# Optimization experiments

Measured on AMD Instinct MI355X. Metric: run time of the kernel, lower is better.

## Reference

```python
import jax, jax.numpy as jnp
import numpy as np

NUM_EMBEDDINGS = 4096
LATENT_DIM = 256
COMMITMENT_COST = 0.25


def setup_inputs() -> dict:
    key = jax.random.key(0)
    k1, k2 = jax.random.split(key)
    x = jax.random.normal(k1, (8, 16, 256, LATENT_DIM), dtype=jnp.float32)
    # codebook initialized uniform(-1/K, 1/K) as in the torch module
    codebook = jax.random.uniform(
        k2, (NUM_EMBEDDINGS, LATENT_DIM), dtype=jnp.float32,
        minval=-1.0 / NUM_EMBEDDINGS, maxval=1.0 / NUM_EMBEDDINGS)
    return {"x": x, "codebook": codebook}


def reference(x, codebook):
    B, T, P, D = x.shape
    z_e = x.reshape(B * T * P, D)                      # [N, D]
    # squared L2 distances: ||z||^2 + ||e||^2 - 2 z.e  -> [N, K]
    z_sq = jnp.sum(z_e * z_e, axis=-1, keepdims=True)  # [N, 1]
    e_sq = jnp.sum(codebook * codebook, axis=-1)       # [K]
    distances = z_sq + e_sq - 2.0 * (z_e @ codebook.T)
    encoding_indices = jnp.argmin(distances, axis=-1)  # [N] int32
    z_q = codebook[encoding_indices].reshape(B, T, P, D)
    # codebook loss + commitment loss (mean squared error)
    loss = jnp.mean((z_q - jax.lax.stop_gradient(x)) ** 2) \
         + COMMITMENT_COST * jnp.mean((jax.lax.stop_gradient(z_q) - x) ** 2)
    # straight-through estimator
    z_q_st = x + jax.lax.stop_gradient(z_q - x)
    return z_q_st, loss, encoding_indices
```

## Files before the change

### kernel.cpp

```cpp
#include <hip/hip_runtime.h>

typedef __attribute__((ext_vector_type(8))) short bf16x8;
typedef __attribute__((ext_vector_type(4))) float f32x4;

#define DIMD 256
#define KCODES 4096
#define NROWS 32768
#define OUT_LOSS 8388608
#define OUT_IDX  8388609
#define MAXC 8
#define EPSQ 40u
#define QSCALE 273066.67f
#define QBIAS  0.12f

struct CandEntry { int row; int cnt; int codes[MAXC]; };

#define WS_CLIST 4096u
#define CCAP     16384
#define WS_OVF   659456u
#define OVFCAP   8192
#define WS_BSW   (1024u*1024u)
#define WS_END   (WS_BSW + (unsigned)KCODES*DIMD*2u)

#define SROWS      128
#define SMEM_WIDX  98816
#define SMEM_WPART 99328
#define SMEM_BYTES 99360

__device__ __forceinline__ unsigned short bf16_rne(float f) {
    unsigned u = __float_as_uint(f);
    u += 0x7FFFu + ((u >> 16) & 1u);
    return (unsigned short)(u >> 16);
}

__device__ __forceinline__ unsigned med3u(unsigned a, unsigned b, unsigned c) {
    unsigned d;
    asm("v_med3_u32 %0, %1, %2, %3" : "=v"(d) : "v"(a), "v"(b), "v"(c));
    return d;
}

__global__ void init_kernel(float* __restrict__ loss_acc, int* __restrict__ wcount,
                            int* __restrict__ ovfcount) {
    if (threadIdx.x == 0) { loss_acc[0] = 0.0f; wcount[0] = 0; ovfcount[0] = 0; }
}

__global__ __launch_bounds__(256) void convertB_kernel(const float* __restrict__ src,
                                                       unsigned short* __restrict__ bsw,
                                                       float* __restrict__ loss_acc,
                                                       int* __restrict__ wcount,
                                                       int* __restrict__ ovfcount,
                                                       int* __restrict__ done) {
    if (blockIdx.x == 0 && threadIdx.x == 0) {
        loss_acc[0] = 0.0f; wcount[0] = 0; ovfcount[0] = 0; done[0] = 0;
    }
    const unsigned u = blockIdx.x * 256 + threadIdx.x;
    const int laneq = u & 3;
    const int kc    = (u >> 2) & 7;
    const int c     = u >> 5;
    const float4 f0 = *(const float4*)(src + (size_t)c * DIMD + kc * 32 + laneq * 8);
    const float4 f1 = *(const float4*)(src + (size_t)c * DIMD + kc * 32 + laneq * 8 + 4);
    ushort4 h0, h1;
    h0.x = bf16_rne(f0.x); h0.y = bf16_rne(f0.y); h0.z = bf16_rne(f0.z); h0.w = bf16_rne(f0.w);
    h1.x = bf16_rne(f1.x); h1.y = bf16_rne(f1.y); h1.z = bf16_rne(f1.z); h1.w = bf16_rne(f1.w);
    const int g = c >> 4, lanem = c & 15;
    unsigned short* dst = bsw + ((size_t)((g * 8 + kc) * 64 + lanem * 4 + laneq)) * 8;
    *(ushort4*)(dst) = h0;
    *(ushort4*)(dst + 4) = h1;
}

__global__ __launch_bounds__(512, 2) void vq_screen_kernel(
        const unsigned short* __restrict__ Bsw,
        const float* __restrict__ x, const float* __restrict__ cb,
        float* __restrict__ out, float* __restrict__ loss_acc,
        int* __restrict__ wcount, CandEntry* __restrict__ clist,
        int* __restrict__ ovfcount, int* __restrict__ ovflist) {
    __shared__ __align__(16) char smem[SMEM_BYTES];
    unsigned short* Asw = (unsigned short*)smem;
    unsigned* keys = (unsigned*)smem;
    int*   widx  = (int*)(smem + SMEM_WIDX);
    float* wpart = (float*)(smem + SMEM_WPART);

    const int tid   = threadIdx.x;
    const int wv    = tid >> 6;
    const int rh    = wv >> 2;
    const int w4    = wv & 3;
    const int lane  = tid & 63;
    const int lanem = lane & 15;
    const int laneq = lane >> 4;
    const int rb    = blockIdx.x * SROWS;
    const int phase = blockIdx.x & 31;

    #pragma unroll
    for (int q = 0; q < 8; ++q) {
        const unsigned u = q * 512 + tid;
        const int lq = u & 3;
        const int kc = (u >> 2) & 7;
        const int rr = u >> 5;
        const float* srcp = x + (size_t)(rb + rr) * DIMD + kc * 32 + lq * 8;
        const float4 f0 = *(const float4*)(srcp);
        const float4 f1 = *(const float4*)(srcp + 4);
        bf16x8 v;
        v[0] = (short)bf16_rne(f0.x); v[1] = (short)bf16_rne(f0.y);
        v[2] = (short)bf16_rne(f0.z); v[3] = (short)bf16_rne(f0.w);
        v[4] = (short)bf16_rne(f1.x); v[5] = (short)bf16_rne(f1.y);
        v[6] = (short)bf16_rne(f1.z); v[7] = (short)bf16_rne(f1.w);
        const int i = rr >> 4, lm = rr & 15;
        *(bf16x8*)(Asw + ((size_t)((i * 8 + kc) * 64 + lq * 16 + lm)) * 8) = v;
    }
    __syncthreads();

    bf16x8 ah[2][8];
    #pragma unroll
    for (int i = 0; i < 2; ++i)
        #pragma unroll
        for (int kc = 0; kc < 8; ++kc)
            ah[i][kc] = *(const bf16x8*)(Asw + (size_t)(((rh * 4 + i) * 8 + kc) * 64 + lane) * 8);

    unsigned b1[16], b2[16], b3[16];
    #pragma unroll
    for (int s = 0; s < 16; ++s) { b1[s] = 0xFFFFFFFFu; b2[s] = 0xFFFFFFFFu; b3[s] = 0xFFFFFFFFu; }

    const int loff = (lanem * 4 + laneq) * 8;

#define LOADH(dst, ctv, jv)                                                       \
    do {                                                                          \
        const int g_ = (ctv) * 8 + w4 * 2 + (jv);                                 \
        _Pragma("unroll")                                                         \
        for (int kc_ = 0; kc_ < 8; ++kc_)                                         \
            dst[kc_] = *(const bf16x8*)(Bsw + (size_t)(g_ * 8 + kc_) * 512 + loff); \
    } while (0)

    bf16x8 bA[8], bB[8];
    LOADH(bA, phase, 0);
    LOADH(bB, phase, 1);

    for (int ct = 0; ct < KCODES / 128; ++ct) {
        const int ctp = (ct + phase) & 31;
        const int ctn = (ctp + 1) & 31;
        f32x4 acc0[4], acc1[4];
        #pragma unroll
        for (int i = 0; i < 4; ++i) {
            acc0[i] = (f32x4){0.f, 0.f, 0.f, 0.f};
            acc1[i] = (f32x4){0.f, 0.f, 0.f, 0.f};
        }

        const int gA = ctn * 8 + w4 * 2 + 0;
        const int gB = ctn * 8 + w4 * 2 + 1;

        #pragma unroll
        for (int kc = 0; kc < 8; ++kc) {
            const bf16x8 a2k = *(const bf16x8*)(Asw + (size_t)(((rh * 4 + 2) * 8 + kc) * 64 + lane) * 8);
            const bf16x8 a3k = *(const bf16x8*)(Asw + (size_t)(((rh * 4 + 3) * 8 + kc) * 64 + lane) * 8);
            acc0[0] = __builtin_amdgcn_mfma_f32_16x16x32_bf16(ah[0][kc], bA[kc], acc0[0], 0, 0, 0);
            acc1[0] = __builtin_amdgcn_mfma_f32_16x16x32_bf16(ah[0][kc], bB[kc], acc1[0], 0, 0, 0);
            acc0[1] = __builtin_amdgcn_mfma_f32_16x16x32_bf16(ah[1][kc], bA[kc], acc0[1], 0, 0, 0);
            acc1[1] = __builtin_amdgcn_mfma_f32_16x16x32_bf16(ah[1][kc], bB[kc], acc1[1], 0, 0, 0);
            acc0[2] = __builtin_amdgcn_mfma_f32_16x16x32_bf16(a2k, bA[kc], acc0[2], 0, 0, 0);
            acc1[2] = __builtin_amdgcn_mfma_f32_16x16x32_bf16(a2k, bB[kc], acc1[2], 0, 0, 0);
            acc0[3] = __builtin_amdgcn_mfma_f32_16x16x32_bf16(a3k, bA[kc], acc0[3], 0, 0, 0);
            acc1[3] = __builtin_amdgcn_mfma_f32_16x16x32_bf16(a3k, bB[kc], acc1[3], 0, 0, 0);
            bA[kc] = *(const bf16x8*)(Bsw + (size_t)(gA * 8 + kc) * 512 + loff);
            bB[kc] = *(const bf16x8*)(Bsw + (size_t)(gB * 8 + kc) * 512 + loff);
            __builtin_amdgcn_sched_barrier(0x38F);
        }

        {
            const unsigned code = (unsigned)(ctp * 128 + w4 * 32 + lanem);
            #pragma unroll
            for (int i = 0; i < 4; ++i)
                #pragma unroll
                for (int r = 0; r < 4; ++r) {
                    const int s = i * 4 + r;
                    const float dist = fmaf(acc0[i][r], -2.0f * QSCALE, QBIAS * QSCALE);
                    const unsigned k = ((unsigned)dist << 12) | code;
                    const unsigned nb1 = min(b1[s], k);
                    const unsigned nb2 = med3u(b1[s], b2[s], k);
                    const unsigned nb3 = med3u(b2[s], b3[s], k);
                    b1[s] = nb1; b2[s] = nb2; b3[s] = nb3;
                }
        }
        {
            const unsigned code = (unsigned)(ctp * 128 + w4 * 32 + 16 + lanem);
            #pragma unroll
            for (int i = 0; i < 4; ++i)
                #pragma unroll
                for (int r = 0; r < 4; ++r) {
                    const int s = i * 4 + r;
                    const float dist = fmaf(acc1[i][r], -2.0f * QSCALE, QBIAS * QSCALE);
                    const unsigned k = ((unsigned)dist << 12) | code;
                    const unsigned nb1 = min(b1[s], k);
                    const unsigned nb2 = med3u(b1[s], b2[s], k);
                    const unsigned nb3 = med3u(b2[s], b3[s], k);
                    b1[s] = nb1; b2[s] = nb2; b3[s] = nb3;
                }
        }
    }
#undef LOADH

    __syncthreads();

    {
        const int src = w4 * 16 + lanem;
        #pragma unroll
        for (int i = 0; i < 4; ++i)
            #pragma unroll
            for (int r = 0; r < 4; ++r) {
                const int s = i * 4 + r;
                const int rr = rh * 64 + i * 16 + laneq * 4 + r;
                keys[rr * 193 + src * 3 + 0] = b1[s];
                keys[rr * 193 + src * 3 + 1] = b2[s];
                keys[rr * 193 + src * 3 + 2] = b3[s];
            }
    }
    __syncthreads();
    if (tid < SROWS) {
        const int base = tid * 193;
        unsigned kmin = 0xFFFFFFFFu;
        for (int t = 0; t < 192; ++t) kmin = min(kmin, keys[base + t]);
        const unsigned thr = (((kmin >> 12) + EPSQ) << 12) | 0xFFFu;
        int cand[MAXC]; int nc = 0; int ovf = 0;
        for (int L = 0; L < 64; ++L) {
            const unsigned v0 = keys[base + L * 3 + 0];
            if (v0 <= thr) {
                if (nc < MAXC) cand[nc] = (int)(v0 & 0xFFFu);
                ++nc;
                const unsigned v1 = keys[base + L * 3 + 1];
                if (v1 <= thr) {
                    if (nc < MAXC) cand[nc] = (int)(v1 & 0xFFFu);
                    ++nc;
                    const unsigned v2 = keys[base + L * 3 + 2];
                    if (v2 <= thr) {
                        if (nc < MAXC) cand[nc] = (int)(v2 & 0xFFFu);
                        ++nc;
                        ovf = 1;
                    }
                }
            }
        }
        const int row = rb + tid;
        const int bi = (int)(kmin & 0xFFFu);
        widx[tid] = bi;
        out[OUT_IDX + (size_t)row] = (float)bi;
        if (ovf || nc > MAXC) {
            const int op = atomicAdd(ovfcount, 1);
            if (op < OVFCAP) ovflist[op] = row;
        } else if (nc >= 2) {
            const int pos = atomicAdd(wcount, 1);
            if (pos < CCAP) {
                CandEntry* e = &clist[pos];
                e->row = row; e->cnt = nc;
                for (int q = 0; q < nc; ++q) e->codes[q] = cand[q];
            } else {
                const int op = atomicAdd(ovfcount, 1);
                if (op < OVFCAP) ovflist[op] = row;
            }
        }
    }
    __syncthreads();

    float lsum = 0.0f;
    const int dv = (tid & 63) * 4;
    const int rs = tid >> 6;
    const float* xblk = x + (size_t)rb * DIMD;
    float* oblk = out + (size_t)rb * DIMD;
    for (int p = 0; p < 16; ++p) {
        const int row = p * 8 + rs;
        const int wi = widx[row];
        float4 xv = *(const float4*)(xblk + (size_t)row * DIMD + dv);
        float4 cv = *(const float4*)(cb + (size_t)wi * DIMD + dv);
        const float d0 = cv.x - xv.x, d1 = cv.y - xv.y, d2 = cv.z - xv.z, d3 = cv.w - xv.w;
        float4 o;
        o.x = xv.x + d0; o.y = xv.y + d1; o.z = xv.z + d2; o.w = xv.w + d3;
        *(float4*)(oblk + (size_t)row * DIMD + dv) = o;
        lsum += d0 * d0 + d1 * d1 + d2 * d2 + d3 * d3;
    }
    #pragma unroll
    for (int off = 32; off > 0; off >>= 1) lsum += __shfl_down(lsum, off, 64);
    if ((tid & 63) == 0) wpart[tid >> 6] = lsum;
    __syncthreads();
    if (tid == 0) {
        float t = 0.0f;
        #pragma unroll
        for (int i = 0; i < 8; ++i) t += wpart[i];
        atomicAdd(loss_acc, t);
    }
}

__global__ __launch_bounds__(256) void vq_fix_kernel(
        const float* __restrict__ x, const float* __restrict__ cb,
        float* __restrict__ out, float* __restrict__ loss_acc,
        const int* __restrict__ wcount, const CandEntry* __restrict__ clist,
        const int* __restrict__ ovfcount, const int* __restrict__ ovflist,
        int* __restrict__ done) {
    __shared__ double xd[DIMD];
    __shared__ double zred[256];
    __shared__ float  rdq[256];
    __shared__ int    ri[256];
    __shared__ float  lred[256];
    const int tid = threadIdx.x;

    {
        int count = wcount[0];
        if (count > CCAP) count = CCAP;
        const int lane = tid & 63;
        const int gw = blockIdx.x * 4 + (tid >> 6);
        const int nw = gridDim.x * 4;
        for (int it = gw; it < count; it += nw) {
            const CandEntry* e = clist + it;
            const int row = e->row;
            const int cnt = e->cnt;
            const float4 xv = *(const float4*)(x + (size_t)row * DIMD + lane * 4);
            double zs = (double)xv.x * xv.x + (double)xv.y * xv.y
                      + (double)xv.z * xv.z + (double)xv.w * xv.w;
            #pragma unroll
            for (int off = 32; off > 0; off >>= 1) zs += __shfl_xor(zs, off, 64);
            const float Zf = (float)zs;
            float bq = 3.4e38f; int bi = 0x7fffffff;
            for (int q = 0; q < cnt; ++q) {
                const int c = e->codes[q];
                const float4 cv = *(const float4*)(cb + (size_t)c * DIMD + lane * 4);
                double dp = (double)xv.x * cv.x + (double)xv.y * cv.y
                          + (double)xv.z * cv.z + (double)xv.w * cv.w;
                #pragma unroll
                for (int off = 32; off > 0; off >>= 1) dp += __shfl_xor(dp, off, 64);
                const float wv = (float)(2.0 * dp);
                const float dq = Zf - wv;
                if (dq < bq || (dq == bq && c < bi)) { bq = dq; bi = c; }
            }
            const int oldi = (int)out[OUT_IDX + (size_t)row];
            if (bi != oldi) {
                const float4 cn = *(const float4*)(cb + (size_t)bi * DIMD + lane * 4);
                const float4 co = *(const float4*)(cb + (size_t)oldi * DIMD + lane * 4);
                float4 o; float ls = 0.0f;
                { const float dn = cn.x - xv.x, dd = co.x - xv.x; o.x = xv.x + dn; ls += dn*dn - dd*dd; }
                { const float dn = cn.y - xv.y, dd = co.y - xv.y; o.y = xv.y + dn; ls += dn*dn - dd*dd; }
                { const float dn = cn.z - xv.z, dd = co.z - xv.z; o.z = xv.z + dn; ls += dn*dn - dd*dd; }
                { const float dn = cn.w - xv.w, dd = co.w - xv.w; o.w = xv.w + dn; ls += dn*dn - dd*dd; }
                *(float4*)(out + (size_t)row * DIMD + lane * 4) = o;
                #pragma unroll
                for (int off = 32; off > 0; off >>= 1) ls += __shfl_xor(ls, off, 64);
                if (lane == 0) {
                    atomicAdd(loss_acc, ls);
                    out[OUT_IDX + (size_t)row] = (float)bi;
                }
            }
        }
    }

    __syncthreads();
    {
        int count = ovfcount[0];
        if (count > OVFCAP) count = OVFCAP;
        for (int item = blockIdx.x; item < count; item += gridDim.x) {
            const int row = ovflist[item];
            const double xv0 = (double)x[(size_t)row * DIMD + tid];
            xd[tid] = xv0;
            zred[tid] = xv0 * xv0;
            __syncthreads();
            for (int st = 128; st > 0; st >>= 1) {
                if (tid < st) zred[tid] += zred[tid + st];
                __syncthreads();
            }
            const float Zf = (float)zred[0];
            float bq = 3.4e38f; int bi = 0x7fffffff;
            for (int q = 0; q < 16; ++q) {
                const int c = q * 256 + tid;
                const float* cr = cb + (size_t)c * DIMD;
                double s0 = 0.0, s1 = 0.0, s2 = 0.0, s3 = 0.0;
                #pragma unroll 4
                for (int d = 0; d < DIMD; d += 16) {
                    float4 c0 = *(const float4*)(cr + d);
                    float4 c1 = *(const float4*)(cr + d + 4);
                    float4 c2 = *(const float4*)(cr + d + 8);
                    float4 c3 = *(const float4*)(cr + d + 12);
                    s0 += xd[d + 0] * (double)c0.x + xd[d + 1] * (double)c0.y
                        + xd[d + 2] * (double)c0.z + xd[d + 3] * (double)c0.w;
                    s1 += xd[d + 4] * (double)c1.x + xd[d + 5] * (double)c1.y
                        + xd[d + 6] * (double)c1.z + xd[d + 7] * (double)c1.w;
                    s2 += xd[d + 8] * (double)c2.x + xd[d + 9] * (double)c2.y
                        + xd[d +10] * (double)c2.z + xd[d +11] * (double)c2.w;
                    s3 += xd[d +12] * (double)c3.x + xd[d +13] * (double)c3.y
                        + xd[d +14] * (double)c3.z + xd[d +15] * (double)c3.w;
                }
                const double s = (s0 + s1) + (s2 + s3);
                const float wv = (float)(2.0 * s);
                const float dq = Zf - wv;
                if (dq < bq || (dq == bq && c < bi)) { bq = dq; bi = c; }
            }
            rdq[tid] = bq; ri[tid] = bi;
            __syncthreads();
            for (int st = 128; st > 0; st >>= 1) {
                if (tid < st) {
                    const float oq = rdq[tid + st]; const int oi = ri[tid + st];
                    if (oq < rdq[tid] || (oq == rdq[tid] && oi < ri[tid])) {
                        rdq[tid] = oq; ri[tid] = oi;
                    }
                }
                __syncthreads();
            }
            const int newi = ri[0];
            const int oldi = (int)out[OUT_IDX + (size_t)row];
            if (newi != oldi) {
                const float xv = x[(size_t)row * DIMD + tid];
                const float co = cb[(size_t)oldi * DIMD + tid];
                const float cn = cb[(size_t)newi * DIMD + tid];
                const float dold = co - xv, dnew = cn - xv;
                out[(size_t)row * DIMD + tid] = xv + dnew;
                lred[tid] = dnew * dnew - dold * dold;
            } else {
                lred[tid] = 0.0f;
            }
            __syncthreads();
            for (int st = 128; st > 0; st >>= 1) {
                if (tid < st) lred[tid] += lred[tid + st];
                __syncthreads();
            }
            if (tid == 0 && newi != oldi) {
                atomicAdd(loss_acc, lred[0]);
                out[OUT_IDX + (size_t)row] = (float)newi;
            }
            __syncthreads();
        }
    }

    __syncthreads();
    if (tid == 0) {
        __threadfence();
        const int t = atomicAdd(done, 1);
        if (t == (int)gridDim.x - 1) {
            __threadfence();
            out[OUT_LOSS] = 1.25f * (loss_acc[0] / 8388608.0f);
        }
    }
}

__global__ __launch_bounds__(256) void vq_ovf_kernel(
        const float* __restrict__ x, const float* __restrict__ cb,
        float* __restrict__ out, float* __restrict__ loss_acc,
        const int* __restrict__ ovfcount, const int* __restrict__ ovflist) {
    __shared__ double xd[DIMD];
    __shared__ double zred[256];
    __shared__ float  rdq[256];
    __shared__ int    ri[256];
    __shared__ float  lred[256];
    const int tid = threadIdx.x;
    int count = ovfcount[0];
    if (count > OVFCAP) count = OVFCAP;
    for (int item = blockIdx.x; item < count; item += gridDim.x) {
        const int row = ovflist[item];
        const double xv0 = (double)x[(size_t)row * DIMD + tid];
        xd[tid] = xv0;
        zred[tid] = xv0 * xv0;
        __syncthreads();
        for (int st = 128; st > 0; st >>= 1) {
            if (tid < st) zred[tid] += zred[tid + st];
            __syncthreads();
        }
        const float Zf = (float)zred[0];
        float bq = 3.4e38f; int bi = 0x7fffffff;
        for (int q = 0; q < 16; ++q) {
            const int c = q * 256 + tid;
            const float* cr = cb + (size_t)c * DIMD;
            double s0 = 0.0, s1 = 0.0, s2 = 0.0, s3 = 0.0;
            #pragma unroll 4
            for (int d = 0; d < DIMD; d += 16) {
                float4 c0 = *(const float4*)(cr + d);
                float4 c1 = *(const float4*)(cr + d + 4);
                float4 c2 = *(const float4*)(cr + d + 8);
                float4 c3 = *(const float4*)(cr + d + 12);
                s0 += xd[d + 0] * (double)c0.x + xd[d + 1] * (double)c0.y
                    + xd[d + 2] * (double)c0.z + xd[d + 3] * (double)c0.w;
                s1 += xd[d + 4] * (double)c1.x + xd[d + 5] * (double)c1.y
                    + xd[d + 6] * (double)c1.z + xd[d + 7] * (double)c1.w;
                s2 += xd[d + 8] * (double)c2.x + xd[d + 9] * (double)c2.y
                    + xd[d +10] * (double)c2.z + xd[d +11] * (double)c2.w;
                s3 += xd[d +12] * (double)c3.x + xd[d +13] * (double)c3.y
                    + xd[d +14] * (double)c3.z + xd[d +15] * (double)c3.w;
            }
            const double s = (s0 + s1) + (s2 + s3);
            const float wv = (float)(2.0 * s);
            const float dq = Zf - wv;
            if (dq < bq || (dq == bq && c < bi)) { bq = dq; bi = c; }
        }
        rdq[tid] = bq; ri[tid] = bi;
        __syncthreads();
        for (int st = 128; st > 0; st >>= 1) {
            if (tid < st) {
                const float oq = rdq[tid + st]; const int oi = ri[tid + st];
                if (oq < rdq[tid] || (oq == rdq[tid] && oi < ri[tid])) {
                    rdq[tid] = oq; ri[tid] = oi;
                }
            }
            __syncthreads();
        }
        const int newi = ri[0];
        const int oldi = (int)out[OUT_IDX + (size_t)row];
        if (newi != oldi) {
            const float xv = x[(size_t)row * DIMD + tid];
            const float co = cb[(size_t)oldi * DIMD + tid];
            const float cn = cb[(size_t)newi * DIMD + tid];
            const float dold = co - xv, dnew = cn - xv;
            out[(size_t)row * DIMD + tid] = xv + dnew;
            lred[tid] = dnew * dnew - dold * dold;
        } else {
            lred[tid] = 0.0f;
        }
        __syncthreads();
        for (int st = 128; st > 0; st >>= 1) {
            if (tid < st) lred[tid] += lred[tid + st];
            __syncthreads();
        }
        if (tid == 0 && newi != oldi) {
            atomicAdd(loss_acc, lred[0]);
            out[OUT_IDX + (size_t)row] = (float)newi;
        }
        __syncthreads();
    }
}

__global__ void finalize_kernel(const float* __restrict__ loss_acc, float* __restrict__ out) {
    if (threadIdx.x == 0 && blockIdx.x == 0)
        out[OUT_LOSS] = 1.25f * (loss_acc[0] / 8388608.0f);
}

#define MT 128
#define DK 32
#define LSTR 130
#define FLAG_EPS_F32 3.6e-5f
__global__ __launch_bounds__(256) void vq_main_fp32_kernel(const float* __restrict__ x,
                                                           const float* __restrict__ cb,
                                                           float* __restrict__ out,
                                                           float* __restrict__ loss_acc,
                                                           int* __restrict__ wcount,
                                                           int* __restrict__ wlist,
                                                           int wcap) {
    __shared__ float As[DK * LSTR];
    __shared__ float Bs[DK * LSTR];
    __shared__ float red_d[MT * 17];
    __shared__ float red_2[MT * 17];
    __shared__ int   red_i[MT * 17];
    __shared__ int   widx[MT];
    __shared__ float wpart[4];
    const int tid = threadIdx.x;
    const int tx = tid & 15;
    const int ty = tid >> 4;
    const float* xblk = x + (size_t)blockIdx.x * MT * DIMD;
    float b1[8], b2[8]; int i1[8];
    #pragma unroll
    for (int i = 0; i < 8; ++i) { b1[i] = 3.4e38f; b2[i] = 3.4e38f; i1[i] = 0; }
    const int sr = tid >> 3;
    const int sd = (tid & 7) * 4;
    for (int kt = 0; kt < KCODES; kt += 128) {
        float acc[8][8];
        #pragma unroll
        for (int i = 0; i < 8; ++i)
            #pragma unroll
            for (int j = 0; j < 8; ++j) acc[i][j] = 0.0f;
        const float* bblk = cb + (size_t)kt * DIMD;
        for (int dc = 0; dc < DIMD; dc += DK) {
            __syncthreads();
            #pragma unroll
            for (int p = 0; p < 4; ++p) {
                const int r = p * 32 + sr;
                float4 va = *(const float4*)(xblk + (size_t)r * DIMD + dc + sd);
                float4 vb = *(const float4*)(bblk + (size_t)r * DIMD + dc + sd);
                As[(sd + 0) * LSTR + r] = va.x; As[(sd + 1) * LSTR + r] = va.y;
                As[(sd + 2) * LSTR + r] = va.z; As[(sd + 3) * LSTR + r] = va.w;
                Bs[(sd + 0) * LSTR + r] = vb.x; Bs[(sd + 1) * LSTR + r] = vb.y;
                Bs[(sd + 2) * LSTR + r] = vb.z; Bs[(sd + 3) * LSTR + r] = vb.w;
            }
            __syncthreads();
            #pragma unroll 4
            for (int d = 0; d < DK; ++d) {
                const float2* ap = (const float2*)&As[d * LSTR + ty * 8];
                const float2* bp = (const float2*)&Bs[d * LSTR + tx * 8];
                float2 a0 = ap[0], a1 = ap[1], a2 = ap[2], a3 = ap[3];
                float2 c0 = bp[0], c1 = bp[1], c2 = bp[2], c3 = bp[3];
                float a[8] = {a0.x, a0.y, a1.x, a1.y, a2.x, a2.y, a3.x, a3.y};
                float b[8] = {c0.x, c0.y, c1.x, c1.y, c2.x, c2.y, c3.x, c3.y};
                #pragma unroll
                for (int i = 0; i < 8; ++i)
                    #pragma unroll
                    for (int j = 0; j < 8; ++j)
                        acc[i][j] += a[i] * b[j];
            }
        }
        #pragma unroll
        for (int j = 0; j < 8; ++j) {
            const int code = kt + tx * 8 + j;
            #pragma unroll
            for (int i = 0; i < 8; ++i) {
                const float dist = -(acc[i][j] + acc[i][j]);
                if (dist < b1[i]) { b2[i] = b1[i]; b1[i] = dist; i1[i] = code; }
                else if (dist < b2[i]) b2[i] = dist;
            }
        }
    }
    __syncthreads();
    #pragma unroll
    for (int i = 0; i < 8; ++i) {
        red_d[(ty * 8 + i) * 17 + tx] = b1[i];
        red_2[(ty * 8 + i) * 17 + tx] = b2[i];
        red_i[(ty * 8 + i) * 17 + tx] = i1[i];
    }
    __syncthreads();
    if (tid < MT) {
        float bd = red_d[tid * 17];
        float s2 = red_2[tid * 17];
        int   bi = red_i[tid * 17];
        #pragma unroll
        for (int t = 1; t < 16; ++t) {
            const float d1 = red_d[tid * 17 + t];
            const float d2 = red_2[tid * 17 + t];
            const int   ii = red_i[tid * 17 + t];
            if (d1 < bd || (d1 == bd && ii < bi)) { s2 = fminf(bd, d2); bd = d1; bi = ii; }
            else s2 = fminf(s2, d1);
        }
        const int row = blockIdx.x * MT + tid;
        widx[tid] = bi;
        out[OUT_IDX + (size_t)row] = (float)bi;
        if (s2 - bd <= FLAG_EPS_F32) {
            const int pos = atomicAdd(wcount, 1);
            if (pos < wcap) wlist[pos] = row;
        }
    }
    __syncthreads();
    float lsum = 0.0f;
    const int dv = (tid & 63) * 4;
    const int rs = tid >> 6;
    float* oblk = out + (size_t)blockIdx.x * MT * DIMD;
    for (int p = 0; p < 32; ++p) {
        const int row = p * 4 + rs;
        const int wi = widx[row];
        float4 xv = *(const float4*)(xblk + (size_t)row * DIMD + dv);
        float4 cv = *(const float4*)(cb + (size_t)wi * DIMD + dv);
        const float d0 = cv.x - xv.x, d1 = cv.y - xv.y, d2 = cv.z - xv.z, d3 = cv.w - xv.w;
        float4 o;
        o.x = xv.x + d0; o.y = xv.y + d1; o.z = xv.z + d2; o.w = xv.w + d3;
        *(float4*)(oblk + (size_t)row * DIMD + dv) = o;
        lsum += d0 * d0 + d1 * d1 + d2 * d2 + d3 * d3;
    }
    #pragma unroll
    for (int off = 32; off > 0; off >>= 1) lsum += __shfl_down(lsum, off, 64);
    if ((tid & 63) == 0) wpart[tid >> 6] = lsum;
    __syncthreads();
    if (tid == 0) atomicAdd(loss_acc, wpart[0] + wpart[1] + wpart[2] + wpart[3]);
}

extern "C" void kernel_launch(void* const* d_in, const int* in_sizes, int n_in,
                              void* d_out, int out_size, void* d_ws, size_t ws_size,
                              hipStream_t stream) {
    const float* x  = (const float*)d_in[0];
    const float* cb = (const float*)d_in[1];
    float* out = (float*)d_out;
    float* loss_acc = (float*)d_ws;
    int*   wcount   = (int*)((char*)d_ws + 32);
    int*   ovfcount = (int*)((char*)d_ws + 36);
    int*   done     = (int*)((char*)d_ws + 40);
    CandEntry* clist = (CandEntry*)((char*)d_ws + WS_CLIST);
    int*   ovflist  = (int*)((char*)d_ws + WS_OVF);

    if (ws_size >= (size_t)WS_END) {
        unsigned short* Bsw = (unsigned short*)((char*)d_ws + WS_BSW);
        convertB_kernel<<<512, 256, 0, stream>>>(cb, Bsw, loss_acc, wcount, ovfcount, done);
        vq_screen_kernel<<<256, 512, 0, stream>>>(Bsw, x, cb, out, loss_acc,
                                                  wcount, clist, ovfcount, ovflist);
        vq_fix_kernel<<<512, 256, 0, stream>>>(x, cb, out, loss_acc,
                                               wcount, clist, ovfcount, ovflist, done);
    } else {
        init_kernel<<<1, 64, 0, stream>>>(loss_acc, wcount, ovfcount);
        int* wlist = (int*)((char*)d_ws + WS_CLIST);
        int wcap = 0;
        if (ws_size > WS_CLIST + sizeof(int)) {
            size_t c = (ws_size - WS_CLIST) / sizeof(int);
            wcap = (int)(c > 32768 ? 32768 : c);
        }
        vq_main_fp32_kernel<<<256, 256, 0, stream>>>(x, cb, out, loss_acc,
                                                     wcount, wlist, wcap);
        vq_ovf_kernel<<<512, 256, 0, stream>>>(x, cb, out, loss_acc, wcount, wlist);
        finalize_kernel<<<1, 1, 0, stream>>>(loss_acc, out);
    }
}
```

Baseline: 193.7 us.

## Fuse candidate rescoring into screen kernel via shared-memory candidate list

The screen kernel now keeps ambiguous-row candidates in a per-block shared-memory list instead of a global list. After the main pass it rescores them in double precision inside the same block, using the indices held in shared memory. The old fix kernel is split, and only the overflow full-search and loss finalize remain in a separate kernel, launched with fewer blocks. This removes global atomics, candidate-list traffic and a heavy kernel stage. In exchange the screen kernel gets a serial tail and a little more shared memory, which may hurt occupancy.

```diff
diff --git a/kernel.cpp b/kernel.cpp
--- a/kernel.cpp
+++ b/kernel.cpp
@@ -25,7 +25,9 @@
 #define SROWS      128
 #define SMEM_WIDX  98816
 #define SMEM_WPART 99328
-#define SMEM_BYTES 99360
+#define SMEM_BCNT  99360
+#define SMEM_CAND  99376
+#define SMEM_BYTES (SMEM_CAND + 128 * 10 * 4)
 
 __device__ __forceinline__ unsigned short bf16_rne(float f) {
     unsigned u = __float_as_uint(f);
@@ -72,13 +74,14 @@
         const unsigned short* __restrict__ Bsw,
         const float* __restrict__ x, const float* __restrict__ cb,
         float* __restrict__ out, float* __restrict__ loss_acc,
-        int* __restrict__ wcount, CandEntry* __restrict__ clist,
         int* __restrict__ ovfcount, int* __restrict__ ovflist) {
     __shared__ __align__(16) char smem[SMEM_BYTES];
     unsigned short* Asw = (unsigned short*)smem;
     unsigned* keys = (unsigned*)smem;
     int*   widx  = (int*)(smem + SMEM_WIDX);
     float* wpart = (float*)(smem + SMEM_WPART);
+    int*   bcnt  = (int*)(smem + SMEM_BCNT);
+    int*   candL = (int*)(smem + SMEM_CAND);
 
     const int tid   = threadIdx.x;
     const int wv    = tid >> 6;
@@ -89,6 +92,8 @@
     const int laneq = lane >> 4;
     const int rb    = blockIdx.x * SROWS;
     const int phase = blockIdx.x & 31;
+
+    if (tid == 0) bcnt[0] = 0;
 
     #pragma unroll
     for (int q = 0; q < 8; ++q) {
@@ -245,15 +250,10 @@
             const int op = atomicAdd(ovfcount, 1);
             if (op < OVFCAP) ovflist[op] = row;
         } else if (nc >= 2) {
-            const int pos = atomicAdd(wcount, 1);
-            if (pos < CCAP) {
-                CandEntry* e = &clist[pos];
-                e->row = row; e->cnt = nc;
-                for (int q = 0; q < nc; ++q) e->codes[q] = cand[q];
-            } else {
-                const int op = atomicAdd(ovfcount, 1);
-                if (op < OVFCAP) ovflist[op] = row;
-            }
+            const int pos = atomicAdd(bcnt, 1);
+            int* e = candL + pos * 10;
+            e[0] = tid; e[1] = nc;
+            for (int q = 0; q < nc; ++q) e[2 + q] = cand[q];
         }
     }
     __syncthreads();
@@ -284,31 +284,15 @@
         for (int i = 0; i < 8; ++i) t += wpart[i];
         atomicAdd(loss_acc, t);
     }
-}
-
-__global__ __launch_bounds__(256) void vq_fix_kernel(
-        const float* __restrict__ x, const float* __restrict__ cb,
-        float* __restrict__ out, float* __restrict__ loss_acc,
-        const int* __restrict__ wcount, const CandEntry* __restrict__ clist,
-        const int* __restrict__ ovfcount, const int* __restrict__ ovflist,
-        int* __restrict__ done) {
-    __shared__ double xd[DIMD];
-    __shared__ double zred[256];
-    __shared__ float  rdq[256];
-    __shared__ int    ri[256];
-    __shared__ float  lred[256];
-    const int tid = threadIdx.x;
+    __syncthreads();
 
     {
-        int count = wcount[0];
-        if (count > CCAP) count = CCAP;
-        const int lane = tid & 63;
-        const int gw = blockIdx.x * 4 + (tid >> 6);
-        const int nw = gridDim.x * 4;
-        for (int it = gw; it < count; it += nw) {
-            const CandEntry* e = clist + it;
-            const int row = e->row;
-            const int cnt = e->cnt;
+        const int items = bcnt[0];
+        for (int it = wv; it < items; it += 8) {
+            const int* e = candL + it * 10;
+            const int r = e[0];
+            const int cnt = e[1];
+            const int row = rb + r;
             const float4 xv = *(const float4*)(x + (size_t)row * DIMD + lane * 4);
             double zs = (double)xv.x * xv.x + (double)xv.y * xv.y
                       + (double)xv.z * xv.z + (double)xv.w * xv.w;
@@ -317,17 +301,17 @@
             const float Zf = (float)zs;
             float bq = 3.4e38f; int bi = 0x7fffffff;
             for (int q = 0; q < cnt; ++q) {
-                const int c = e->codes[q];
+                const int c = e[2 + q];
                 const float4 cv = *(const float4*)(cb + (size_t)c * DIMD + lane * 4);
                 double dp = (double)xv.x * cv.x + (double)xv.y * cv.y
                           + (double)xv.z * cv.z + (double)xv.w * cv.w;
                 #pragma unroll
                 for (int off = 32; off > 0; off >>= 1) dp += __shfl_xor(dp, off, 64);
-                const float wv = (float)(2.0 * dp);
-                const float dq = Zf - wv;
+                const float wvv = (float)(2.0 * dp);
+                const float dq = Zf - wvv;
                 if (dq < bq || (dq == bq && c < bi)) { bq = dq; bi = c; }
             }
-            const int oldi = (int)out[OUT_IDX + (size_t)row];
+            const int oldi = widx[r];
             if (bi != oldi) {
                 const float4 cn = *(const float4*)(cb + (size_t)bi * DIMD + lane * 4);
                 const float4 co = *(const float4*)(cb + (size_t)oldi * DIMD + lane * 4);
@@ -346,84 +330,91 @@
             }
         }
     }
-
-    __syncthreads();
-    {
-        int count = ovfcount[0];
-        if (count > OVFCAP) count = OVFCAP;
-        for (int item = blockIdx.x; item < count; item += gridDim.x) {
-            const int row = ovflist[item];
-            const double xv0 = (double)x[(size_t)row * DIMD + tid];
-            xd[tid] = xv0;
-            zred[tid] = xv0 * xv0;
-            __syncthreads();
-            for (int st = 128; st > 0; st >>= 1) {
-                if (tid < st) zred[tid] += zred[tid + st];
-                __syncthreads();
-            }
-            const float Zf = (float)zred[0];
-            float bq = 3.4e38f; int bi = 0x7fffffff;
-            for (int q = 0; q < 16; ++q) {
-                const int c = q * 256 + tid;
-                const float* cr = cb + (size_t)c * DIMD;
-                double s0 = 0.0, s1 = 0.0, s2 = 0.0, s3 = 0.0;
-                #pragma unroll 4
-                for (int d = 0; d < DIMD; d += 16) {
-                    float4 c0 = *(const float4*)(cr + d);
-                    float4 c1 = *(const float4*)(cr + d + 4);
-                    float4 c2 = *(const float4*)(cr + d + 8);
-                    float4 c3 = *(const float4*)(cr + d + 12);
-                    s0 += xd[d + 0] * (double)c0.x + xd[d + 1] * (double)c0.y
-                        + xd[d + 2] * (double)c0.z + xd[d + 3] * (double)c0.w;
-                    s1 += xd[d + 4] * (double)c1.x + xd[d + 5] * (double)c1.y
-                        + xd[d + 6] * (double)c1.z + xd[d + 7] * (double)c1.w;
-                    s2 += xd[d + 8] * (double)c2.x + xd[d + 9] * (double)c2.y
-                        + xd[d +10] * (double)c2.z + xd[d +11] * (double)c2.w;
-                    s3 += xd[d +12] * (double)c3.x + xd[d +13] * (double)c3.y
-                        + xd[d +14] * (double)c3.z + xd[d +15] * (double)c3.w;
+}
+
+__global__ __launch_bounds__(256) void vq_ovffin_kernel(
+        const float* __restrict__ x, const float* __restrict__ cb,
+        float* __restrict__ out, float* __restrict__ loss_acc,
+        const int* __restrict__ ovfcount, const int* __restrict__ ovflist,
+        int* __restrict__ done) {
+    __shared__ double xd[DIMD];
+    __shared__ double zred[256];
+    __shared__ float  rdq[256];
+    __shared__ int    ri[256];
+    __shared__ float  lred[256];
+    const int tid = threadIdx.x;
+    int count = ovfcount[0];
+    if (count > OVFCAP) count = OVFCAP;
+    for (int item = blockIdx.x; item < count; item += gridDim.x) {
+        const int row = ovflist[item];
+        const double xv0 = (double)x[(size_t)row * DIMD + tid];
+        xd[tid] = xv0;
+        zred[tid] = xv0 * xv0;
+        __syncthreads();
+        for (int st = 128; st > 0; st >>= 1) {
+            if (tid < st) zred[tid] += zred[tid + st];
+            __syncthreads();
+        }
+        const float Zf = (float)zred[0];
+        float bq = 3.4e38f; int bi = 0x7fffffff;
+        for (int q = 0; q < 16; ++q) {
+            const int c = q * 256 + tid;
+            const float* cr = cb + (size_t)c * DIMD;
+            double s0 = 0.0, s1 = 0.0, s2 = 0.0, s3 = 0.0;
+            #pragma unroll 4
+            for (int d = 0; d < DIMD; d += 16) {
+                float4 c0 = *(const float4*)(cr + d);
+                float4 c1 = *(const float4*)(cr + d + 4);
+                float4 c2 = *(const float4*)(cr + d + 8);
+                float4 c3 = *(const float4*)(cr + d + 12);
+                s0 += xd[d + 0] * (double)c0.x + xd[d + 1] * (double)c0.y
+                    + xd[d + 2] * (double)c0.z + xd[d + 3] * (double)c0.w;
+                s1 += xd[d + 4] * (double)c1.x + xd[d + 5] * (double)c1.y
+                    + xd[d + 6] * (double)c1.z + xd[d + 7] * (double)c1.w;
+                s2 += xd[d + 8] * (double)c2.x + xd[d + 9] * (double)c2.y
+                    + xd[d +10] * (double)c2.z + xd[d +11] * (double)c2.w;
+                s3 += xd[d +12] * (double)c3.x + xd[d +13] * (double)c3.y
+                    + xd[d +14] * (double)c3.z + xd[d +15] * (double)c3.w;
+            }
+            const double s = (s0 + s1) + (s2 + s3);
+            const float wv = (float)(2.0 * s);
+            const float dq = Zf - wv;
+            if (dq < bq || (dq == bq && c < bi)) { bq = dq; bi = c; }
+        }
+        rdq[tid] = bq; ri[tid] = bi;
+        __syncthreads();
+        for (int st = 128; st > 0; st >>= 1) {
+            if (tid < st) {
+                const float oq = rdq[tid + st]; const int oi = ri[tid + st];
+                if (oq < rdq[tid] || (oq == rdq[tid] && oi < ri[tid])) {
+                    rdq[tid] = oq; ri[tid] = oi;
                 }
-                const double s = (s0 + s1) + (s2 + s3);
-                const float wv = (float)(2.0 * s);
-                const float dq = Zf - wv;
-                if (dq < bq || (dq == bq && c < bi)) { bq = dq; bi = c; }
-            }
-            rdq[tid] = bq; ri[tid] = bi;
-            __syncthreads();
-            for (int st = 128; st > 0; st >>= 1) {
-                if (tid < st) {
-                    const float oq = rdq[tid + st]; const int oi = ri[tid + st];
-                    if (oq < rdq[tid] || (oq == rdq[tid] && oi < ri[tid])) {
-                        rdq[tid] = oq; ri[tid] = oi;
-                    }
-                }
-                __syncthreads();
-            }
-            const int newi = ri[0];
-            const int oldi = (int)out[OUT_IDX + (size_t)row];
-            if (newi != oldi) {
-                const float xv = x[(size_t)row * DIMD + tid];
-                const float co = cb[(size_t)oldi * DIMD + tid];
-                const float cn = cb[(size_t)newi * DIMD + tid];
-                const float dold = co - xv, dnew = cn - xv;
-                out[(size_t)row * DIMD + tid] = xv + dnew;
-                lred[tid] = dnew * dnew - dold * dold;
-            } else {
-                lred[tid] = 0.0f;
-            }
-            __syncthreads();
-            for (int st = 128; st > 0; st >>= 1) {
-                if (tid < st) lred[tid] += lred[tid + st];
-                __syncthreads();
-            }
-            if (tid == 0 && newi != oldi) {
-                atomicAdd(loss_acc, lred[0]);
-                out[OUT_IDX + (size_t)row] = (float)newi;
-            }
-            __syncthreads();
-        }
-    }
-
-    __syncthreads();
+            }
+            __syncthreads();
+        }
+        const int newi = ri[0];
+        const int oldi = (int)out[OUT_IDX + (size_t)row];
+        if (newi != oldi) {
+            const float xv = x[(size_t)row * DIMD + tid];
+            const float co = cb[(size_t)oldi * DIMD + tid];
+            const float cn = cb[(size_t)newi * DIMD + tid];
+            const float dold = co - xv, dnew = cn - xv;
+            out[(size_t)row * DIMD + tid] = xv + dnew;
+            lred[tid] = dnew * dnew - dold * dold;
+        } else {
+            lred[tid] = 0.0f;
+        }
+        __syncthreads();
+        for (int st = 128; st > 0; st >>= 1) {
+            if (tid < st) lred[tid] += lred[tid + st];
+            __syncthreads();
+        }
+        if (tid == 0 && newi != oldi) {
+            atomicAdd(loss_acc, lred[0]);
+            out[OUT_IDX + (size_t)row] = (float)newi;
+        }
+        __syncthreads();
+    }
     if (tid == 0) {
         __threadfence();
         const int t = atomicAdd(done, 1);
@@ -657,16 +648,15 @@
     int*   wcount   = (int*)((char*)d_ws + 32);
     int*   ovfcount = (int*)((char*)d_ws + 36);
     int*   done     = (int*)((char*)d_ws + 40);
-    CandEntry* clist = (CandEntry*)((char*)d_ws + WS_CLIST);
     int*   ovflist  = (int*)((char*)d_ws + WS_OVF);
 
     if (ws_size >= (size_t)WS_END) {
         unsigned short* Bsw = (unsigned short*)((char*)d_ws + WS_BSW);
         convertB_kernel<<<512, 256, 0, stream>>>(cb, Bsw, loss_acc, wcount, ovfcount, done);
         vq_screen_kernel<<<256, 512, 0, stream>>>(Bsw, x, cb, out, loss_acc,
-                                                  wcount, clist, ovfcount, ovflist);
-        vq_fix_kernel<<<512, 256, 0, stream>>>(x, cb, out, loss_acc,
-                                               wcount, clist, ovfcount, ovflist, done);
+                                                  ovfcount, ovflist);
+        vq_ovffin_kernel<<<256, 256, 0, stream>>>(x, cb, out, loss_acc,
+                                                  ovfcount, ovflist, done);
     } else {
         init_kernel<<<1, 64, 0, stream>>>(loss_acc, wcount, ovfcount);
         int* wlist = (int*)((char*)d_ws + WS_CLIST);
```

Measured after the change: 183.3 us. 5.4% less time.
